# Kernel optimization log

Measured on AMD Instinct MI355X. Metric: run time of the kernel, lower is better.

Reference implementation:

```python
import jax, jax.numpy as jnp
import numpy as np

IN_FEATURES = 16384
OUT_FEATURES = 16384
NNZ = 1_000_000
BATCH = 256


def setup_inputs() -> dict:
    key = jax.random.key(0)
    k_x, k_w, k_b, k_r, k_c = jax.random.split(key, 5)
    x = jax.random.normal(k_x, (BATCH, IN_FEATURES), dtype=jnp.float32)
    weight_vals = jax.random.normal(k_w, (NNZ,), dtype=jnp.float32)
    bias = jax.random.normal(k_b, (OUT_FEATURES,), dtype=jnp.float32)
    rows = jax.random.randint(k_r, (NNZ,), 0, OUT_FEATURES, dtype=jnp.int32)
    cols = jax.random.randint(k_c, (NNZ,), 0, IN_FEATURES, dtype=jnp.int32)
    return {"x": x, "weight_vals": weight_vals, "bias": bias,
            "rows": rows, "cols": cols}


def reference(x, weight_vals, bias, rows, cols):
    # SparseLinear forward: y = x @ W^T + b, with W sparse COO of shape
    # [out_features, in_features]; (rows, cols) are W's nnz coordinates.
    # Per-edge contribution: x[:, col] * W[row, col], scattered into out[:, row].
    contrib = x[:, cols] * weight_vals  # [B, nnz]
    # segment-sum edges into output features: [nnz, B] -> [out, B]
    out = jax.ops.segment_sum(contrib.T, rows, num_segments=OUT_FEATURES).T
    return out + bias  # [B, out_features]
```

## Files before the change

kernel.cpp:

```cpp
#include <hip/hip_runtime.h>
#include <hip/hip_bf16.h>
#include <hip/hip_fp16.h>

#define IN_F    16384
#define OUT_F   16384
#define CAP     128
#define NBUCK   512
#define CAPB    2560
#define EPB     4096
#define TBLK    1024

typedef unsigned int u32x4 __attribute__((ext_vector_type(4)));
typedef float f32x4 __attribute__((ext_vector_type(4)));


__global__ void prep_kernel(const float* __restrict__ x,
                            __hip_bfloat16* __restrict__ xTh,
                            const int* __restrict__ rows,
                            const int* __restrict__ cols,
                            const float* __restrict__ vals, int nnz, int npart,
                            int* __restrict__ gcursor,
                            uint2* __restrict__ staging) {
    __shared__ __align__(16) union {
        float tile[64 * 65];
        struct {
            uint2 recs[EPB];
            int hist[NBUCK];
            int lstart[NBUCK];
            int gbase[NBUCK];
            int scanbuf[256];
        } pa;
    } sm;
    int t = threadIdx.x;
    if ((int)blockIdx.x < npart) {
        sm.pa.hist[t] = 0; sm.pa.hist[t + 256] = 0;
        __syncthreads();
        int i0 = blockIdx.x * EPB;
        unsigned int pk[16], vb[16];
#pragma unroll
        for (int k = 0; k < 16; ++k) {
            int i = i0 + k * 256 + t;
            if (i < nnz) {
                int r = rows[i], c = cols[i];
                pk[k] = ((unsigned int)r << 14) | (unsigned int)c;
                vb[k] = ((unsigned int)c << 16) |
                        (unsigned int)__half_as_ushort(__float2half(vals[i]));
                atomicAdd(&sm.pa.hist[r >> 5], 1);
            } else pk[k] = 0xffffffffu;
        }
        __syncthreads();
        int h0 = sm.pa.hist[2 * t], h1 = sm.pa.hist[2 * t + 1];
        sm.pa.scanbuf[t] = h0 + h1;
        __syncthreads();
        for (int off = 1; off < 256; off <<= 1) {
            int add = (t >= off) ? sm.pa.scanbuf[t - off] : 0;
            __syncthreads();
            sm.pa.scanbuf[t] += add;
            __syncthreads();
        }
        int excl = sm.pa.scanbuf[t] - (h0 + h1);
        sm.pa.lstart[2 * t]     = excl;
        sm.pa.lstart[2 * t + 1] = excl + h0;
        sm.pa.gbase[2 * t]     = h0 > 0 ? atomicAdd(&gcursor[2 * t], h0) : 0;
        sm.pa.gbase[2 * t + 1] = h1 > 0 ? atomicAdd(&gcursor[2 * t + 1], h1) : 0;
        __syncthreads();
        sm.pa.hist[t] = 0; sm.pa.hist[t + 256] = 0;
        __syncthreads();
#pragma unroll
        for (int k = 0; k < 16; ++k) {
            if (pk[k] != 0xffffffffu) {
                int b = pk[k] >> 19;
                int pos = sm.pa.lstart[b] + atomicAdd(&sm.pa.hist[b], 1);
                sm.pa.recs[pos] = make_uint2(pk[k], vb[k]);
            }
        }
        __syncthreads();
        int total = sm.pa.scanbuf[255];
        for (int j = t; j < total; j += 256) {
            uint2 rec = sm.pa.recs[j];
            int b = rec.x >> 19;
            int gp = sm.pa.gbase[b] + (j - sm.pa.lstart[b]);
            if (gp < CAPB) {
                unsigned long long pv =
                    (unsigned long long)rec.x | ((unsigned long long)rec.y << 32);
                __builtin_nontemporal_store(pv,
                    (unsigned long long*)(staging + (size_t)b * CAPB + gp));
            }
        }
    } else {
        float* tile = (float*)&sm;
        int bid = blockIdx.x - npart;
        int i0 = (bid & 255) * 64;
        int b0 = (bid >> 8) * 64;
        int tx4 = t & 15;
        int r16 = t >> 4;
#pragma unroll
        for (int k = 0; k < 4; ++k) {
            int row = r16 + k * 16;
            f32x4 v = *(const f32x4*)(x + (size_t)(b0 + row) * IN_F + i0 + tx4 * 4);
            tile[row * 65 + tx4 * 4 + 0] = v.x;
            tile[row * 65 + tx4 * 4 + 1] = v.y;
            tile[row * 65 + tx4 * 4 + 2] = v.z;
            tile[row * 65 + tx4 * 4 + 3] = v.w;
        }
        __syncthreads();
        int tx = t & 63, ty = t >> 6;
        int h = b0 >> 7, j0 = b0 & 127;
#pragma unroll
        for (int k = 0; k < 64; k += 4) {
            int col = i0 + ty + k;
            xTh[((size_t)h * IN_F + col) * 128 + j0 + tx] =
                __float2bfloat16(tile[tx * 65 + ty + k]);
        }
    }
}


__global__ void __launch_bounds__(512, 6)
accum_kernel(const unsigned int* __restrict__ xh0,
             const uint2* __restrict__ staging,
             const int* __restrict__ gcursor,
             const float* __restrict__ bias,
             float* __restrict__ out) {
    __shared__ union {
        unsigned int lbin[32 * CAP];
        float slab[32 * 129];
    } u;
    __shared__ int lcnt[32];
    int blk = blockIdx.x;
    int h = blk & 1;
    int bu = blk >> 1;
    int o0 = bu * 32;
    int t = threadIdx.x;
    int w = t >> 6, lane = t & 63;
    {
        u32x4 z = {0u, 0u, 0u, 0u};
#pragma unroll
        for (int i = 0; i < 2; ++i)
            *(u32x4*)&u.lbin[(t + i * 512) * 4] = z;
    }
    if (t < 32) lcnt[t] = 0;
    __syncthreads();
    int n = gcursor[bu];
    if (n > CAPB) n = CAPB;
    const unsigned long long* st = (const unsigned long long*)(staging + (size_t)bu * CAPB);
    for (int i = t; i < n; i += 512) {
        unsigned long long v = __builtin_nontemporal_load(st + i);
        unsigned int rx = (unsigned int)v;
        unsigned int ry = (unsigned int)(v >> 32);
        int rl = (rx >> 14) & 31;
        int p = atomicAdd(&lcnt[rl], 1);
        if (p < CAP) u.lbin[rl * CAP + p] = ry;
    }
    __syncthreads();
    const unsigned int* xh = xh0 + (size_t)h * IN_F * 64;
    int rl0 = w * 4;
    int c0 = lcnt[rl0 + 0]; if (c0 > CAP) c0 = CAP;
    int c1 = lcnt[rl0 + 1]; if (c1 > CAP) c1 = CAP;
    int c2 = lcnt[rl0 + 2]; if (c2 > CAP) c2 = CAP;
    int c3 = lcnt[rl0 + 3]; if (c3 > CAP) c3 = CAP;
    int cm01 = c0 > c1 ? c0 : c1;
    int cm23 = c2 > c3 ? c2 : c3;
    int cm = cm01 > cm23 ? cm01 : cm23;
    int lim = (cm + 3) & ~3;
    const u32x4* lb0 = (const u32x4*)&u.lbin[(rl0 + 0) * CAP];
    const u32x4* lb1 = (const u32x4*)&u.lbin[(rl0 + 1) * CAP];
    const u32x4* lb2 = (const u32x4*)&u.lbin[(rl0 + 2) * CAP];
    const u32x4* lb3 = (const u32x4*)&u.lbin[(rl0 + 3) * CAP];
    float aa[4] = {0.f, 0.f, 0.f, 0.f};
    float ab[4] = {0.f, 0.f, 0.f, 0.f};
    if (lim > 0) {
        u32x4 cu0 = lb0[0], cu1 = lb1[0], cu2 = lb2[0], cu3 = lb3[0];
        for (int j = 0; j < lim; j += 4) {
            int jn = (j >> 2) + 1;
            u32x4 nx0 = lb0[jn], nx1 = lb1[jn];
            u32x4 nx2 = lb2[jn], nx3 = lb3[jn];
            unsigned int e[16] = {cu0.x, cu0.y, cu0.z, cu0.w,
                                  cu1.x, cu1.y, cu1.z, cu1.w,
                                  cu2.x, cu2.y, cu2.z, cu2.w,
                                  cu3.x, cu3.y, cu3.z, cu3.w};
            unsigned int s[16], g[16];
#pragma unroll
            for (int k = 0; k < 16; ++k) {
                s[k] = __builtin_amdgcn_readfirstlane(e[k]);
                g[k] = *(xh + ((s[k] >> 16) << 6) + lane);
            }
#pragma unroll
            for (int r = 0; r < 4; ++r) {
#pragma unroll
                for (int k = 0; k < 4; ++k) {
                    int q = r * 4 + k;
                    float v = __half2float(__ushort_as_half(
                                  (unsigned short)(s[q] & 0xffffu)));
                    aa[r] += __uint_as_float(g[q] << 16) * v;
                    ab[r] += __uint_as_float(g[q] & 0xffff0000u) * v;
                }
            }
            cu0 = nx0; cu1 = nx1; cu2 = nx2; cu3 = nx3;
        }
    }
    __syncthreads();
#pragma unroll
    for (int rr = 0; rr < 4; ++rr) {
        int rl = rl0 + rr;
        u.slab[rl * 129 + 2 * lane + 0] = aa[rr];
        u.slab[rl * 129 + 2 * lane + 1] = ab[rr];
    }
    __syncthreads();
#pragma unroll
    for (int it = 0; it < 2; ++it) {
        int item = t + it * 512;
        int bl = item >> 3;
        int q = item & 7;
        f32x4 bv = *(const f32x4*)(bias + o0 + q * 4);
        f32x4 v;
        v.x = u.slab[(q * 4 + 0) * 129 + bl] + bv.x;
        v.y = u.slab[(q * 4 + 1) * 129 + bl] + bv.y;
        v.z = u.slab[(q * 4 + 2) * 129 + bl] + bv.z;
        v.w = u.slab[(q * 4 + 3) * 129 + bl] + bv.w;
        __builtin_nontemporal_store(v,
            (f32x4*)(out + (size_t)(h * 128 + bl) * OUT_F + o0 + q * 4));
    }
}

extern "C" void kernel_launch(void* const* d_in, const int* in_sizes, int n_in,
                              void* d_out, int out_size, void* d_ws, size_t ws_size,
                              hipStream_t stream) {
    const float* x     = (const float*)d_in[0];
    const float* wvals = (const float*)d_in[1];
    const float* bias  = (const float*)d_in[2];
    const int*   rows  = (const int*)d_in[3];
    const int*   cols  = (const int*)d_in[4];
    float* out = (float*)d_out;
    int nnz = in_sizes[1];

    const size_t MB = 1024 * 1024;
    char* ws = (char*)d_ws;
    __hip_bfloat16* xTh = (__hip_bfloat16*)(ws);
    uint2* staging = (uint2*)(ws + 8 * MB);
    int*   gcursor = (int*)(ws + 20 * MB);

    (void)hipMemsetAsync(gcursor, 0, NBUCK * sizeof(int), stream);

    int npart = (nnz + EPB - 1) / EPB;
    prep_kernel<<<npart + TBLK, 256, 0, stream>>>(x, xTh, rows, cols, wvals, nnz,
                                                  npart, gcursor, staging);
    accum_kernel<<<NBUCK * 2, 512, 0, stream>>>((const unsigned int*)xTh, staging,
                                                gcursor, bias, out);
}
```

Before: 135.4 us.

## Halve prep partition size, use wave-shuffle scan, pack accumulators as float2

```diff
diff --git a/kernel.cpp b/kernel.cpp
--- a/kernel.cpp
+++ b/kernel.cpp
@@ -7,11 +7,12 @@
 #define CAP     128
 #define NBUCK   512
 #define CAPB    2560
-#define EPB     4096
+#define EPB     2048
 #define TBLK    1024
 
 typedef unsigned int u32x4 __attribute__((ext_vector_type(4)));
 typedef float f32x4 __attribute__((ext_vector_type(4)));
+typedef float f32x2 __attribute__((ext_vector_type(2)));
 
 
 __global__ void prep_kernel(const float* __restrict__ x,
@@ -28,7 +29,8 @@
             int hist[NBUCK];
             int lstart[NBUCK];
             int gbase[NBUCK];
-            int scanbuf[256];
+            int wsum[4];
+            int total;
         } pa;
     } sm;
     int t = threadIdx.x;
@@ -36,9 +38,9 @@
         sm.pa.hist[t] = 0; sm.pa.hist[t + 256] = 0;
         __syncthreads();
         int i0 = blockIdx.x * EPB;
-        unsigned int pk[16], vb[16];
-#pragma unroll
-        for (int k = 0; k < 16; ++k) {
+        unsigned int pk[8], vb[8];
+#pragma unroll
+        for (int k = 0; k < 8; ++k) {
             int i = i0 + k * 256 + t;
             if (i < nnz) {
                 int r = rows[i], c = cols[i];
@@ -49,25 +51,31 @@
             } else pk[k] = 0xffffffffu;
         }
         __syncthreads();
+        int lane = t & 63, w = t >> 6;
         int h0 = sm.pa.hist[2 * t], h1 = sm.pa.hist[2 * t + 1];
-        sm.pa.scanbuf[t] = h0 + h1;
-        __syncthreads();
-        for (int off = 1; off < 256; off <<= 1) {
-            int add = (t >= off) ? sm.pa.scanbuf[t - off] : 0;
-            __syncthreads();
-            sm.pa.scanbuf[t] += add;
-            __syncthreads();
-        }
-        int excl = sm.pa.scanbuf[t] - (h0 + h1);
+        int pv = h0 + h1;
+        int incl = pv;
+#pragma unroll
+        for (int off = 1; off < 64; off <<= 1) {
+            int u = __shfl_up(incl, off, 64);
+            if (lane >= off) incl += u;
+        }
+        if (lane == 63) sm.pa.wsum[w] = incl;
+        __syncthreads();
+        int addw = 0;
+#pragma unroll
+        for (int q = 0; q < 3; ++q) addw += (q < w) ? sm.pa.wsum[q] : 0;
+        incl += addw;
+        int excl = incl - pv;
         sm.pa.lstart[2 * t]     = excl;
         sm.pa.lstart[2 * t + 1] = excl + h0;
         sm.pa.gbase[2 * t]     = h0 > 0 ? atomicAdd(&gcursor[2 * t], h0) : 0;
         sm.pa.gbase[2 * t + 1] = h1 > 0 ? atomicAdd(&gcursor[2 * t + 1], h1) : 0;
-        __syncthreads();
+        if (t == 255) sm.pa.total = incl;
         sm.pa.hist[t] = 0; sm.pa.hist[t + 256] = 0;
         __syncthreads();
 #pragma unroll
-        for (int k = 0; k < 16; ++k) {
+        for (int k = 0; k < 8; ++k) {
             if (pk[k] != 0xffffffffu) {
                 int b = pk[k] >> 19;
                 int pos = sm.pa.lstart[b] + atomicAdd(&sm.pa.hist[b], 1);
@@ -75,15 +83,15 @@
             }
         }
         __syncthreads();
-        int total = sm.pa.scanbuf[255];
+        int total = sm.pa.total;
         for (int j = t; j < total; j += 256) {
             uint2 rec = sm.pa.recs[j];
             int b = rec.x >> 19;
             int gp = sm.pa.gbase[b] + (j - sm.pa.lstart[b]);
             if (gp < CAPB) {
-                unsigned long long pv =
+                unsigned long long pvv =
                     (unsigned long long)rec.x | ((unsigned long long)rec.y << 32);
-                __builtin_nontemporal_store(pv,
+                __builtin_nontemporal_store(pvv,
                     (unsigned long long*)(staging + (size_t)b * CAPB + gp));
             }
         }
@@ -116,7 +124,7 @@
 }
 
 
-__global__ void __launch_bounds__(512, 6)
+__global__ void __launch_bounds__(512, 4)
 accum_kernel(const unsigned int* __restrict__ xh0,
              const uint2* __restrict__ staging,
              const int* __restrict__ gcursor,
@@ -143,7 +151,8 @@
     __syncthreads();
     int n = gcursor[bu];
     if (n > CAPB) n = CAPB;
-    const unsigned long long* st = (const unsigned long long*)(staging + (size_t)bu * CAPB);
+    const unsigned long long* st =
+        (const unsigned long long*)(staging + (size_t)bu * CAPB);
     for (int i = t; i < n; i += 512) {
         unsigned long long v = __builtin_nontemporal_load(st + i);
         unsigned int rx = (unsigned int)v;
@@ -167,8 +176,9 @@
     const u32x4* lb1 = (const u32x4*)&u.lbin[(rl0 + 1) * CAP];
     const u32x4* lb2 = (const u32x4*)&u.lbin[(rl0 + 2) * CAP];
     const u32x4* lb3 = (const u32x4*)&u.lbin[(rl0 + 3) * CAP];
-    float aa[4] = {0.f, 0.f, 0.f, 0.f};
-    float ab[4] = {0.f, 0.f, 0.f, 0.f};
+    f32x2 acc[4];
+#pragma unroll
+    for (int r = 0; r < 4; ++r) acc[r] = (f32x2){0.f, 0.f};
     if (lim > 0) {
         u32x4 cu0 = lb0[0], cu1 = lb1[0], cu2 = lb2[0], cu3 = lb3[0];
         for (int j = 0; j < lim; j += 4) {
@@ -190,10 +200,13 @@
 #pragma unroll
                 for (int k = 0; k < 4; ++k) {
                     int q = r * 4 + k;
-                    float v = __half2float(__ushort_as_half(
-                                  (unsigned short)(s[q] & 0xffffu)));
-                    aa[r] += __uint_as_float(g[q] << 16) * v;
-                    ab[r] += __uint_as_float(g[q] & 0xffff0000u) * v;
+                    float vv = __half2float(__ushort_as_half(
+                                   (unsigned short)(s[q] & 0xffffu)));
+                    f32x2 m;
+                    m.x = __uint_as_float(g[q] << 16);
+                    m.y = __uint_as_float(g[q] & 0xffff0000u);
+                    f32x2 v2 = {vv, vv};
+                    acc[r] += m * v2;
                 }
             }
             cu0 = nx0; cu1 = nx1; cu2 = nx2; cu3 = nx3;
@@ -203,8 +216,8 @@
 #pragma unroll
     for (int rr = 0; rr < 4; ++rr) {
         int rl = rl0 + rr;
-        u.slab[rl * 129 + 2 * lane + 0] = aa[rr];
-        u.slab[rl * 129 + 2 * lane + 1] = ab[rr];
+        u.slab[rl * 129 + 2 * lane + 0] = acc[rr].x;
+        u.slab[rl * 129 + 2 * lane + 1] = acc[rr].y;
     }
     __syncthreads();
 #pragma unroll
```

Measured after the change: 146.2 us. +8.0%, slower.
